# Kernel tuning notes

Measured on AMD Instinct MI355X. Metric: run time of the kernel, lower is better.

The kernel has to match this reference:

```python
import jax, jax.numpy as jnp
import numpy as np

D = 512   # embed_dim
K = 8     # expand_dim
TAU = 16.0
LN_EPS = 1e-5


def setup_inputs() -> dict:
    key = jax.random.key(0)
    ks = jax.random.split(key, 8)
    b, n = 4, 4096
    x = jax.random.normal(ks[0], (b, n, D), dtype=jnp.float32)
    # nn.Linear weights stored as (in, out); bias=False everywhere
    W_i = jax.random.normal(ks[1], (D, D), dtype=jnp.float32) / np.sqrt(D)
    W_e = jax.random.normal(ks[2], (D, K), dtype=jnp.float32) / np.sqrt(D)
    W_s = jax.random.normal(ks[3], (D, K), dtype=jnp.float32) / np.sqrt(D)
    o_param = jax.random.normal(ks[4], (K, D), dtype=jnp.float32) * 0.1
    ln_gamma = jnp.ones((D,), dtype=jnp.float32)
    ln_beta = jnp.zeros((D,), dtype=jnp.float32)
    W_out = jax.random.normal(ks[5], (D, D), dtype=jnp.float32) / np.sqrt(D)
    return {"x": x, "W_i": W_i, "W_e": W_e, "W_s": W_s, "o_param": o_param,
            "ln_gamma": ln_gamma, "ln_beta": ln_beta, "W_out": W_out}


def reference(x, W_i, W_e, W_s, o_param, ln_gamma, ln_beta, W_out):
    b, n, d = x.shape
    k = W_e.shape[1]
    i = x @ W_i            # (b,n,d) input branch
    e = x @ W_e            # (b,n,k) expand branch (t_type=0: identity)
    s = x @ W_s            # (b,n,k) shrink branch
    # data-independent decay gate: exp(logsigmoid(o)/tau), shape (k,d)
    o = jnp.exp(jax.nn.log_sigmoid(o_param) / TAU)

    def step(m, inp):
        it, et, st = inp          # (b,d), (b,k), (b,k)
        m = o * m + et[:, :, None] * it[:, None, :]   # (b,k,d)
        y = jnp.einsum('bk,bkd->bd', st, m)
        return m, y

    m0 = jnp.zeros((b, k, d), dtype=x.dtype)
    xs = (jnp.swapaxes(i, 0, 1), jnp.swapaxes(e, 0, 1), jnp.swapaxes(s, 0, 1))
    _, ys = jax.lax.scan(step, m0, xs)   # ys: (n,b,d)
    y = jnp.swapaxes(ys, 0, 1)           # (b,n,d)
    # LayerNorm
    mu = jnp.mean(y, axis=-1, keepdims=True)
    var = jnp.mean(jnp.square(y - mu), axis=-1, keepdims=True)
    y = (y - mu) * jax.lax.rsqrt(var + LN_EPS) * ln_gamma + ln_beta
    return y @ W_out
```

## Files before the change

kernel.cpp:

```cpp
#include <hip/hip_runtime.h>
#include <stdint.h>

typedef __bf16 bf16;
typedef __bf16 bf16x8 __attribute__((ext_vector_type(8)));
typedef float  f32x4  __attribute__((ext_vector_type(4)));

#define NSEQ 4096
#define NROWS 16384
#define CHUNK 32
#define NCHUNKS_B 128
#define NCHUNKS 512
#define SEGLEN 16
#define NSEG 8
#define YSTRIDE 516

__device__ __forceinline__ float bf2f(uint16_t u){
    uint32_t w = ((uint32_t)u) << 16;
    return __builtin_bit_cast(float, w);
}
__device__ __forceinline__ uint32_t pack2(float a, float b){
    uint16_t ua = __builtin_bit_cast(uint16_t, (bf16)a);
    uint16_t ub = __builtin_bit_cast(uint16_t, (bf16)b);
    return ((uint32_t)ub << 16) | (uint32_t)ua;
}
__device__ __forceinline__ uint4 cvt8(const float* p){
    float4 lo = *(const float4*)p;
    float4 hi = *(const float4*)(p + 4);
    uint4 r;
    r.x = pack2(lo.x, lo.y); r.y = pack2(lo.z, lo.w);
    r.z = pack2(hi.x, hi.y); r.w = pack2(hi.z, hi.w);
    return r;
}
__device__ __forceinline__ float rd_any(const void* p, long idx, int f){
    return f ? ((const float*)p)[idx] : (float)((const bf16*)p)[idx];
}
__device__ __forceinline__ void cp16(const void* g, void* l){
    __builtin_amdgcn_global_load_lds((const __attribute__((address_space(1))) void*)g,
                                     (__attribute__((address_space(3))) void*)l,
                                     16, 0, 0);
}

__global__ __launch_bounds__(256) void prep_all(const uint32_t* __restrict__ xw,
                                                const void* __restrict__ Wi,
                                                const void* __restrict__ Wo,
                                                const void* We, const void* Ws,
                                                const void* op, const void* g, const void* bta,
                                                bf16* __restrict__ Wt_i, bf16* __restrict__ Wt_o,
                                                bf16* __restrict__ Wt_es,
                                                float* __restrict__ g_c, float* __restrict__ b_c,
                                                float* __restrict__ o_buf, float* __restrict__ oL_buf,
                                                float* __restrict__ lsL_buf, float* __restrict__ oL16_buf,
                                                int* __restrict__ flag_g){
    __shared__ int cnt[256];
    __shared__ bf16 T[64][65];
    int tid = threadIdx.x;
    int c = 0;
    #pragma unroll
    for (int j = 0; j < 4; ++j){
        uint32_t w = xw[tid*4 + j];
        uint32_t e = (w >> 7) & 0xFF;
        c += (e >= 110 && e <= 140) ? 1 : 0;
    }
    cnt[tid] = c; __syncthreads();
    for (int s = 128; s; s >>= 1){
        if (tid < s) cnt[tid] += cnt[tid + s];
        __syncthreads();
    }
    int f = (cnt[0] < 512) ? 1 : 0;
    int blk = blockIdx.x;
    if (blk == 0 && tid == 0) flag_g[0] = f;

    if (blk < 128){
        int mat = blk >> 6;
        int t   = blk & 63;
        int k0  = (t >> 3) * 64, n0 = (t & 7) * 64;
        const void* in = mat ? Wo : Wi;
        bf16* out = mat ? Wt_o : Wt_i;
        #pragma unroll
        for (int e = 0; e < 16; ++e){
            int idx = e*256 + tid;
            int r = idx >> 6, cc = idx & 63;
            T[cc][r] = (bf16)rd_any(in, (long)(k0 + r)*512 + n0 + cc, f);
        }
        __syncthreads();
        #pragma unroll
        for (int e = 0; e < 16; ++e){
            int idx = e*256 + tid;
            int rn = idx >> 6, ck = idx & 63;
            out[(long)(n0 + rn)*512 + k0 + ck] = T[rn][ck];
        }
    } else if (blk < 136){
        int sub = blk - 128;
        for (int i = tid; i < 1024; i += 256){
            int gi = sub*1024 + i;
            int n = gi >> 9, k = gi & 511;
            float v = (n < 8) ? rd_any(We, (long)k*8 + n, f)
                              : rd_any(Ws, (long)k*8 + (n-8), f);
            Wt_es[gi] = (bf16)v;
        }
    } else {
        int sub = blk - 136;
        int base = sub * 1024;
        for (int i = tid; i < 1024; i += 256){
            int gi = base + i;
            float x = rd_any(op, gi, f);
            float ls = (x < 0.f) ? (x - log1pf(expf(x))) : (0.f - log1pf(expf(-x)));
            o_buf[gi]    = expf(ls * (1.0f/16.0f));
            oL_buf[gi]   = expf(ls * 2.0f);
            lsL_buf[gi]  = ls * 2.0f;
            oL16_buf[gi] = expf(ls * 32.0f);
        }
        if (sub == 0){
            for (int i = tid; i < 512; i += 256){
                g_c[i] = rd_any(g, i, f);
                b_c[i] = rd_any(bta, i, f);
            }
        }
    }
}

__global__ __launch_bounds__(256) void gemm_bt(const void* __restrict__ Avoid,
                                               const bf16* __restrict__ Bt,
                                               void* __restrict__ Cvoid,
                                               int M, int N, int Kd,
                                               const int* __restrict__ aflag,
                                               const int* __restrict__ cflag,
                                               const bf16* __restrict__ Wes,
                                               float* __restrict__ e_out,
                                               float* __restrict__ s_out,
                                               float* __restrict__ Ams,
                                               const float* __restrict__ o_buf){
    __shared__ __align__(16) char smem[36*1024];
    bf16*  As = (bf16*)smem;
    bf16*  Bs = (bf16*)(smem + 16384);
    bf16*  iT = (bf16*)smem;
    float* eS = (float*)(smem + 32768);
    const int tid  = threadIdx.x;
    const int lane = tid & 63;
    const int wave = tid >> 6;
    const int ntiles = N >> 7;
    int bid = blockIdx.x;
    {
        const int q = gridDim.x >> 3;
        bid = (bid & 7) * q + (bid >> 3);
    }
    const int mtile = bid / ntiles;
    const int ntile = bid - mtile*ntiles;
    const int m0 = mtile << 7, n0 = ntile << 7;
    const int wr = (wave >> 1) << 6;
    const int wc = (wave & 1) << 6;
    const int lrow = lane & 15;
    const int quad = lane >> 4;
    const int fa = aflag ? *aflag : 0;
    const bool do_es = (Wes != nullptr) && ((wave & 1) == 0);

    f32x4 acc[4][4] = {};
    f32x4 acc_es[4] = {};

    const int sr = tid >> 2;
    const int sk = (tid & 3) << 3;
    const bf16*  Ag  = (const bf16*) Avoid + (long)(m0 + sr)*Kd + sk;
    const float* Agf = (const float*)Avoid + (long)(m0 + sr)*Kd + sk;
    const bf16*  Bg  = Bt + (long)(n0 + sr)*Kd + sk;

    if (fa){
        *(uint4*)&As[tid*8]        = cvt8(Agf);
        *(uint4*)&As[2048 + tid*8] = cvt8(Agf + (long)64*Kd);
    } else {
        cp16(Ag,                 As + (size_t)wave*512);
        cp16(Ag + (long)64*Kd,   As + 2048 + (size_t)wave*512);
    }
    cp16(Bg,               Bs + (size_t)wave*512);
    cp16(Bg + (long)64*Kd, Bs + 2048 + (size_t)wave*512);
    __syncthreads();

    int cur = 0;
    for (int k0 = 0; k0 < Kd; k0 += 32){
        const int nxt  = cur ^ 1;
        const int k1   = k0 + 32;
        const bool more = (k1 < Kd);
        float4 la0, la1, lb0, lb1;
        if (more){
            if (fa){
                la0 = *(const float4*)(Agf + k1);
                la1 = *(const float4*)(Agf + k1 + 4);
                lb0 = *(const float4*)(Agf + (long)64*Kd + k1);
                lb1 = *(const float4*)(Agf + (long)64*Kd + k1 + 4);
            } else {
                cp16(Ag + k1,               As + nxt*4096 + (size_t)wave*512);
                cp16(Ag + (long)64*Kd + k1, As + nxt*4096 + 2048 + (size_t)wave*512);
            }
            cp16(Bg + k1,               Bs + nxt*4096 + (size_t)wave*512);
            cp16(Bg + (long)64*Kd + k1, Bs + nxt*4096 + 2048 + (size_t)wave*512);
        }

        bf16x8 af[4], bfr[4];
        #pragma unroll
        for (int i = 0; i < 4; ++i)
            af[i]  = *(const bf16x8*)&As[cur*4096 + (wr + i*16 + lrow)*32 + quad*8];
        #pragma unroll
        for (int j = 0; j < 4; ++j)
            bfr[j] = *(const bf16x8*)&Bs[cur*4096 + (wc + j*16 + lrow)*32 + quad*8];
        #pragma unroll
        for (int i = 0; i < 4; ++i)
            #pragma unroll
            for (int j = 0; j < 4; ++j)
                acc[i][j] = __builtin_amdgcn_mfma_f32_16x16x32_bf16(af[i], bfr[j], acc[i][j], 0, 0, 0);
        if (do_es){
            bf16x8 be = *(const bf16x8*)(Wes + (long)lrow*512 + k0 + quad*8);
            #pragma unroll
            for (int i = 0; i < 4; ++i)
                acc_es[i] = __builtin_amdgcn_mfma_f32_16x16x32_bf16(af[i], be, acc_es[i], 0, 0, 0);
        }

        if (more && fa){
            uint4 A0, A1;
            A0.x = pack2(la0.x, la0.y); A0.y = pack2(la0.z, la0.w);
            A0.z = pack2(la1.x, la1.y); A0.w = pack2(la1.z, la1.w);
            A1.x = pack2(lb0.x, lb0.y); A1.y = pack2(lb0.z, lb0.w);
            A1.z = pack2(lb1.x, lb1.y); A1.w = pack2(lb1.z, lb1.w);
            *(uint4*)&As[nxt*4096 + tid*8]        = A0;
            *(uint4*)&As[nxt*4096 + 2048 + tid*8] = A1;
        }
        __syncthreads();
        cur = nxt;
    }

    const int fc = cflag ? *cflag : 0;
    if (fc){
        float* Cf = (float*)Cvoid;
        #pragma unroll
        for (int i = 0; i < 4; ++i){
            int gr = m0 + wr + i*16 + quad*4;
            #pragma unroll
            for (int j = 0; j < 4; ++j){
                int gc = n0 + wc + j*16 + lrow;
                #pragma unroll
                for (int r = 0; r < 4; ++r)
                    Cf[(long)(gr + r)*N + gc] = acc[i][j][r];
            }
        }
    } else {
        bf16* Cb = (bf16*)Cvoid;
        #pragma unroll
        for (int i = 0; i < 4; ++i){
            int gr = m0 + wr + i*16 + quad*4;
            #pragma unroll
            for (int j = 0; j < 4; ++j){
                int gc = n0 + wc + j*16 + lrow;
                #pragma unroll
                for (int r = 0; r < 4; ++r)
                    Cb[(long)(gr + r)*N + gc] = (bf16)acc[i][j][r];
            }
        }
    }
    if (do_es && ntile == 0){
        float* eo = (lrow < 8) ? e_out : s_out;
        int col = lrow & 7;
        #pragma unroll
        for (int i = 0; i < 4; ++i){
            int gr = m0 + wr + i*16 + quad*4;
            #pragma unroll
            for (int r = 0; r < 4; ++r)
                eo[(long)(gr + r)*8 + col] = acc_es[i][r];
        }
    }

    if (Ams){
        #pragma unroll
        for (int i = 0; i < 4; ++i){
            int lr = wr + i*16 + quad*4;
            #pragma unroll
            for (int j = 0; j < 4; ++j){
                int lc = wc + j*16 + lrow;
                #pragma unroll
                for (int r = 0; r < 4; ++r)
                    iT[(lr + r)*128 + lc] = (bf16)acc[i][j][r];
            }
        }
        if (do_es && lrow < 8){
            #pragma unroll
            for (int i = 0; i < 4; ++i){
                int lr = wr + i*16 + quad*4;
                #pragma unroll
                for (int r = 0; r < 4; ++r)
                    eS[(lr + r)*8 + lrow] = acc_es[i][r];
            }
        }
        __syncthreads();
        const int dp  = tid & 63;
        const int kq  = tid >> 6;
        const int dl  = dp*2;
        const int ki  = kq*2;
        const float o00 = o_buf[(ki  )*512 + n0 + dl];
        const float o01 = o_buf[(ki  )*512 + n0 + dl + 1];
        const float o10 = o_buf[(ki+1)*512 + n0 + dl];
        const float o11 = o_buf[(ki+1)*512 + n0 + dl + 1];
        #pragma unroll
        for (int c = 0; c < 4; ++c){
            float m00 = 0.f, m01 = 0.f, m10 = 0.f, m11 = 0.f;
            for (int t = 0; t < CHUNK; ++t){
                int row = c*32 + t;
                uint32_t iv = *(const uint32_t*)&iT[row*128 + dl];
                float i0 = bf2f((uint16_t)iv), i1 = bf2f((uint16_t)(iv >> 16));
                float e0 = eS[row*8 + ki], e1 = eS[row*8 + ki + 1];
                m00 = o00*m00 + e0*i0;  m01 = o01*m01 + e0*i1;
                m10 = o10*m10 + e1*i0;  m11 = o11*m11 + e1*i1;
            }
            float* Ac = Ams + (long)((m0 >> 5) + c)*4096 + n0 + dl;
            float2 v0; v0.x = m00; v0.y = m01;
            float2 v1; v1.x = m10; v1.y = m11;
            *(float2*)&Ac[(ki  )*512] = v0;
            *(float2*)&Ac[(ki+1)*512] = v1;
        }
    }
}

__global__ __launch_bounds__(256) void passB1(float* __restrict__ Ams,
                                              const float* __restrict__ oL_buf,
                                              float* __restrict__ Tbuf){
    int bs  = blockIdx.x >> 4;
    int b   = bs >> 3, seg = bs & 7;
    int idx = (blockIdx.x & 15)*256 + threadIdx.x;
    float oL = oL_buf[idx];
    float m = 0.f;
    float* Mb = Ams + ((long)b*NCHUNKS_B + seg*SEGLEN)*4096 + idx;
    #pragma unroll 4
    for (int cc = 0; cc < SEGLEN; ++cc){
        float a = Mb[(long)cc*4096];
        Mb[(long)cc*4096] = m;
        m = oL*m + a;
    }
    Tbuf[(long)bs*4096 + idx] = m;
}

__global__ __launch_bounds__(256) void passC(bf16* __restrict__ iy,
                                             const float* __restrict__ e_buf,
                                             const float* __restrict__ s_buf,
                                             const float* __restrict__ o_buf,
                                             const float* __restrict__ Ploc,
                                             const float* __restrict__ Tbuf,
                                             const float* __restrict__ lsL_buf,
                                             const float* __restrict__ oL16_buf,
                                             const float* __restrict__ g_c,
                                             const float* __restrict__ b_c){
    int c  = blockIdx.x;
    int b  = c >> 7;
    int cI = c & 127;
    int seg = cI >> 4;
    float fj = (float)(cI & 15);
    int t0 = cI * CHUNK;
    int tid = threadIdx.x;
    __shared__ float eS[CHUNK*8], sS[CHUNK*8];
    __shared__ float muS[CHUNK], rS[CHUNK];
    __shared__ __align__(16) float yS[CHUNK][YSTRIDE];
    eS[tid] = e_buf[((long)(b*NSEQ + t0))*8 + tid];
    sS[tid] = s_buf[((long)(b*NSEQ + t0))*8 + tid];
    __syncthreads();
    int d0 = tid*2;
    float o0[8], o1[8], m0[8], m1[8];
    const float* P0 = Ploc + (long)c*4096;
    #pragma unroll
    for (int k = 0; k < 8; ++k){
        int i0 = k*512 + d0;
        float ms0 = 0.f, ms1 = 0.f;
        float w0 = oL16_buf[i0], w1 = oL16_buf[i0+1];
        for (int u = 0; u < seg; ++u){
            const float* T = Tbuf + ((long)(b*NSEG + u))*4096;
            ms0 = w0*ms0 + T[i0];
            ms1 = w1*ms1 + T[i0+1];
        }
        o0[k] = o_buf[i0]; o1[k] = o_buf[i0 + 1];
        m0[k] = P0[i0]   + __expf(lsL_buf[i0]  *fj)*ms0;
        m1[k] = P0[i0+1] + __expf(lsL_buf[i0+1]*fj)*ms1;
    }
    bf16* ip = iy + (long)(b*NSEQ + t0)*512 + d0;
    for (int t = 0; t < CHUNK; ++t){
        uint32_t iv = *(const uint32_t*)(ip + (long)t*512);
        float i0 = bf2f((uint16_t)iv), i1 = bf2f((uint16_t)(iv >> 16));
        float y0 = 0.f, y1 = 0.f;
        #pragma unroll
        for (int k = 0; k < 8; ++k){
            float ek = eS[t*8 + k], sk = sS[t*8 + k];
            m0[k] = o0[k]*m0[k] + ek*i0;
            m1[k] = o1[k]*m1[k] + ek*i1;
            y0 += sk*m0[k];
            y1 += sk*m1[k];
        }
        float2 yv; yv.x = y0; yv.y = y1;
        *(float2*)&yS[t][d0] = yv;
    }
    __syncthreads();
    {
        int row = tid >> 3, sub = tid & 7;
        const float4* yr = (const float4*)&yS[row][sub*64];
        float s = 0.f, s2 = 0.f;
        #pragma unroll
        for (int j = 0; j < 16; ++j){
            float4 v = yr[j];
            s  += v.x + v.y + v.z + v.w;
            s2 += v.x*v.x + v.y*v.y + v.z*v.z + v.w*v.w;
        }
        s += __shfl_xor(s, 1); s2 += __shfl_xor(s2, 1);
        s += __shfl_xor(s, 2); s2 += __shfl_xor(s2, 2);
        s += __shfl_xor(s, 4); s2 += __shfl_xor(s2, 4);
        if (sub == 0){
            float mu  = s * (1.f/512.f);
            float var = s2 * (1.f/512.f) - mu*mu;
            muS[row] = mu;
            rS[row]  = rsqrtf(var + 1e-5f);
        }
    }
    __syncthreads();
    float g0 = g_c[d0], g1 = g_c[d0+1];
    float bb0 = b_c[d0], bb1 = b_c[d0+1];
    for (int t = 0; t < CHUNK; ++t){
        float mu = muS[t], r = rS[t];
        float2 yv = *(const float2*)&yS[t][d0];
        float a0 = (yv.x - mu)*r*g0 + bb0;
        float a1 = (yv.y - mu)*r*g1 + bb1;
        *(uint32_t*)(ip + (long)t*512) = pack2(a0, a1);
    }
}

extern "C" void kernel_launch(void* const* d_in, const int* in_sizes, int n_in,
                              void* d_out, int out_size, void* d_ws, size_t ws_size,
                              hipStream_t stream){
    const void* x    = d_in[0];
    const void* W_i  = d_in[1];
    const void* W_e  = d_in[2];
    const void* W_s  = d_in[3];
    const void* o_p  = d_in[4];
    const void* gmm  = d_in[5];
    const void* bta  = d_in[6];
    const void* W_o  = d_in[7];

    char* ws = (char*)d_ws;
    bf16*  Wt_i   = (bf16*) (ws + 0);
    float* Tbuf   = (float*)(ws + 0);
    bf16*  Wt_o   = (bf16*) (ws + 524288);
    bf16*  iy_buf = (bf16*) (ws + 1048576);
    float* e_buf  = (float*)(ws + 17825792);
    float* s_buf  = (float*)(ws + 18350080);
    float* o_buf  = (float*)(ws + 18874368);
    float* oL_buf = (float*)(ws + 18890752);
    float* lsL    = (float*)(ws + 18907136);
    float* oL16   = (float*)(ws + 18923520);
    float* Ams    = (float*)(ws + 18939904);
    bf16*  Wt_es  = (bf16*) (ws + 27328512);
    float* g_c    = (float*)(ws + 27344896);
    float* b_c    = (float*)(ws + 27346944);
    int*   flag   = (int*)  (ws + 27348992);

    prep_all<<<140, 256, 0, stream>>>((const uint32_t*)x, W_i, W_o, W_e, W_s, o_p, gmm, bta,
                                      Wt_i, Wt_o, Wt_es, g_c, b_c, o_buf, oL_buf, lsL, oL16, flag);
    gemm_bt <<<512, 256, 0, stream>>>(x, Wt_i, iy_buf, NROWS, 512, 512, flag, nullptr,
                                      Wt_es, e_buf, s_buf, Ams, o_buf);
    passB1 <<<512,  256, 0, stream>>>(Ams, oL_buf, Tbuf);
    passC  <<<NCHUNKS, 256, 0, stream>>>(iy_buf, e_buf, s_buf, o_buf, Ams, Tbuf, lsL,
                                         oL16, g_c, b_c);
    gemm_bt <<<512, 256, 0, stream>>>(iy_buf, Wt_o, d_out, NROWS, 512, 512, nullptr, flag,
                                      nullptr, nullptr, nullptr, nullptr, nullptr);
}
```

Baseline: 173.4 us.

## Fuse output projection GEMM into scan/LayerNorm kernel using MFMA

The chunked scan kernel now keeps its LayerNorm-ed outputs in shared memory as bf16 and multiplies them directly by W_out with MFMA instructions, writing the final output. The separate output GEMM launch and the global round trip of the normalized activations are removed. The y values are now rounded to bf16 before the LayerNorm statistics are computed, which loses some precision. The fused GEMM loads W_out fragments straight from global memory with no shared-memory tiling, which may be less efficient than the dedicated GEMM kernel.

```diff
diff --git a/kernel.cpp b/kernel.cpp
--- a/kernel.cpp
+++ b/kernel.cpp
@@ -12,7 +12,7 @@
 #define NCHUNKS 512
 #define SEGLEN 16
 #define NSEG 8
-#define YSTRIDE 516
+#define YST2 520
 
 __device__ __forceinline__ float bf2f(uint16_t u){
     uint32_t w = ((uint32_t)u) << 16;
@@ -334,16 +334,19 @@
     Tbuf[(long)bs*4096 + idx] = m;
 }
 
-__global__ __launch_bounds__(256) void passC(bf16* __restrict__ iy,
-                                             const float* __restrict__ e_buf,
-                                             const float* __restrict__ s_buf,
-                                             const float* __restrict__ o_buf,
-                                             const float* __restrict__ Ploc,
-                                             const float* __restrict__ Tbuf,
-                                             const float* __restrict__ lsL_buf,
-                                             const float* __restrict__ oL16_buf,
-                                             const float* __restrict__ g_c,
-                                             const float* __restrict__ b_c){
+__global__ __launch_bounds__(256) void passCG(const bf16* __restrict__ iy,
+                                              const float* __restrict__ e_buf,
+                                              const float* __restrict__ s_buf,
+                                              const float* __restrict__ o_buf,
+                                              const float* __restrict__ Ploc,
+                                              const float* __restrict__ Tbuf,
+                                              const float* __restrict__ lsL_buf,
+                                              const float* __restrict__ oL16_buf,
+                                              const float* __restrict__ g_c,
+                                              const float* __restrict__ b_c,
+                                              const bf16* __restrict__ Wt_o,
+                                              void* __restrict__ outp,
+                                              const int* __restrict__ cflag){
     int c  = blockIdx.x;
     int b  = c >> 7;
     int cI = c & 127;
@@ -351,9 +354,13 @@
     float fj = (float)(cI & 15);
     int t0 = cI * CHUNK;
     int tid = threadIdx.x;
+    const int lane = tid & 63;
+    const int wave = tid >> 6;
+    const int lrow = lane & 15;
+    const int quad = lane >> 4;
     __shared__ float eS[CHUNK*8], sS[CHUNK*8];
     __shared__ float muS[CHUNK], rS[CHUNK];
-    __shared__ __align__(16) float yS[CHUNK][YSTRIDE];
+    __shared__ __align__(16) bf16 yB[CHUNK * YST2];
     eS[tid] = e_buf[((long)(b*NSEQ + t0))*8 + tid];
     sS[tid] = s_buf[((long)(b*NSEQ + t0))*8 + tid];
     __syncthreads();
@@ -374,7 +381,7 @@
         m0[k] = P0[i0]   + __expf(lsL_buf[i0]  *fj)*ms0;
         m1[k] = P0[i0+1] + __expf(lsL_buf[i0+1]*fj)*ms1;
     }
-    bf16* ip = iy + (long)(b*NSEQ + t0)*512 + d0;
+    const bf16* ip = iy + (long)(b*NSEQ + t0)*512 + d0;
     for (int t = 0; t < CHUNK; ++t){
         uint32_t iv = *(const uint32_t*)(ip + (long)t*512);
         float i0 = bf2f((uint16_t)iv), i1 = bf2f((uint16_t)(iv >> 16));
@@ -387,24 +394,26 @@
             y0 += sk*m0[k];
             y1 += sk*m1[k];
         }
-        float2 yv; yv.x = y0; yv.y = y1;
-        *(float2*)&yS[t][d0] = yv;
+        *(uint32_t*)&yB[t*YST2 + d0] = pack2(y0, y1);
     }
     __syncthreads();
-    {
-        int row = tid >> 3, sub = tid & 7;
-        const float4* yr = (const float4*)&yS[row][sub*64];
+    #pragma unroll
+    for (int rr = 0; rr < 8; ++rr){
+        int row = wave*8 + rr;
+        uint4 u = *(const uint4*)&yB[row*YST2 + lane*8];
+        const uint16_t* uu = (const uint16_t*)&u;
         float s = 0.f, s2 = 0.f;
         #pragma unroll
-        for (int j = 0; j < 16; ++j){
-            float4 v = yr[j];
-            s  += v.x + v.y + v.z + v.w;
-            s2 += v.x*v.x + v.y*v.y + v.z*v.z + v.w*v.w;
-        }
-        s += __shfl_xor(s, 1); s2 += __shfl_xor(s2, 1);
-        s += __shfl_xor(s, 2); s2 += __shfl_xor(s2, 2);
-        s += __shfl_xor(s, 4); s2 += __shfl_xor(s2, 4);
-        if (sub == 0){
+        for (int j = 0; j < 8; ++j){
+            float v = bf2f(uu[j]);
+            s += v; s2 += v*v;
+        }
+        #pragma unroll
+        for (int off = 1; off < 64; off <<= 1){
+            s  += __shfl_xor(s, off);
+            s2 += __shfl_xor(s2, off);
+        }
+        if (lane == 0){
             float mu  = s * (1.f/512.f);
             float var = s2 * (1.f/512.f) - mu*mu;
             muS[row] = mu;
@@ -412,14 +421,61 @@
         }
     }
     __syncthreads();
-    float g0 = g_c[d0], g1 = g_c[d0+1];
-    float bb0 = b_c[d0], bb1 = b_c[d0+1];
-    for (int t = 0; t < CHUNK; ++t){
-        float mu = muS[t], r = rS[t];
-        float2 yv = *(const float2*)&yS[t][d0];
-        float a0 = (yv.x - mu)*r*g0 + bb0;
-        float a1 = (yv.y - mu)*r*g1 + bb1;
-        *(uint32_t*)(ip + (long)t*512) = pack2(a0, a1);
+    {
+        float g0 = g_c[d0], g1 = g_c[d0+1];
+        float bb0 = b_c[d0], bb1 = b_c[d0+1];
+        for (int t = 0; t < CHUNK; ++t){
+            float mu = muS[t], r = rS[t];
+            uint32_t yv = *(const uint32_t*)&yB[t*YST2 + d0];
+            float a0 = (bf2f((uint16_t)yv)         - mu)*r*g0 + bb0;
+            float a1 = (bf2f((uint16_t)(yv >> 16)) - mu)*r*g1 + bb1;
+            *(uint32_t*)&yB[t*YST2 + d0] = pack2(a0, a1);
+        }
+    }
+    __syncthreads();
+    {
+        const int col0 = wave*128;
+        f32x4 acc[2][8] = {};
+        for (int k0 = 0; k0 < 512; k0 += 32){
+            bf16x8 af[2];
+            #pragma unroll
+            for (int i = 0; i < 2; ++i)
+                af[i] = *(const bf16x8*)&yB[(i*16 + lrow)*YST2 + k0 + quad*8];
+            #pragma unroll
+            for (int j = 0; j < 8; ++j){
+                bf16x8 bfr = *(const bf16x8*)(Wt_o + (long)(col0 + j*16 + lrow)*512 + k0 + quad*8);
+                #pragma unroll
+                for (int i = 0; i < 2; ++i)
+                    acc[i][j] = __builtin_amdgcn_mfma_f32_16x16x32_bf16(af[i], bfr, acc[i][j], 0, 0, 0);
+            }
+        }
+        const long rowb = (long)(b*NSEQ + t0);
+        const int fc = cflag ? *cflag : 0;
+        if (fc){
+            float* Cf = (float*)outp;
+            #pragma unroll
+            for (int i = 0; i < 2; ++i){
+                #pragma unroll
+                for (int j = 0; j < 8; ++j){
+                    int gc = col0 + j*16 + lrow;
+                    #pragma unroll
+                    for (int r = 0; r < 4; ++r)
+                        Cf[(rowb + i*16 + quad*4 + r)*512 + gc] = acc[i][j][r];
+                }
+            }
+        } else {
+            bf16* Cb = (bf16*)outp;
+            #pragma unroll
+            for (int i = 0; i < 2; ++i){
+                #pragma unroll
+                for (int j = 0; j < 8; ++j){
+                    int gc = col0 + j*16 + lrow;
+                    #pragma unroll
+                    for (int r = 0; r < 4; ++r)
+                        Cb[(rowb + i*16 + quad*4 + r)*512 + gc] = (bf16)acc[i][j][r];
+                }
+            }
+        }
     }
 }
 
@@ -457,8 +513,6 @@
     gemm_bt <<<512, 256, 0, stream>>>(x, Wt_i, iy_buf, NROWS, 512, 512, flag, nullptr,
                                       Wt_es, e_buf, s_buf, Ams, o_buf);
     passB1 <<<512,  256, 0, stream>>>(Ams, oL_buf, Tbuf);
-    passC  <<<NCHUNKS, 256, 0, stream>>>(iy_buf, e_buf, s_buf, o_buf, Ams, Tbuf, lsL,
-                                         oL16, g_c, b_c);
-    gemm_bt <<<512, 256, 0, stream>>>(iy_buf, Wt_o, d_out, NROWS, 512, 512, nullptr, flag,
-                                      nullptr, nullptr, nullptr, nullptr, nullptr);
-}
+    passCG <<<NCHUNKS, 256, 0, stream>>>(iy_buf, e_buf, s_buf, o_buf, Ams, Tbuf, lsL,
+                                         oL16, g_c, b_c, Wt_o, d_out, flag);
+}
```

Result: slower. 192.3 us (+10.9%).
